# Kernel tuning notes

Hardware: AMD Instinct MI355X
Metric: run time of the kernel (lower is better)

## Reference

```python
import jax, jax.numpy as jnp
import numpy as np

N0, N1, N2 = 60000, 30000, 15000
E1, E2 = 960000, 480000
G, D, C = 2000, 400, 20
S0, S1, S2 = 1000, 1500, 2000  # gene index slice boundaries (shared/human/mouse)
EPS = 1e-5


def setup_inputs() -> dict:
    key = jax.random.key(0)
    ks = jax.random.split(key, 30)
    def lin(k, o, i):
        return (jax.random.normal(k, (o, i), jnp.float32) / np.sqrt(i)).astype(jnp.float32)
    inp = {}
    inp['x'] = jax.random.normal(ks[0], (N0, G), jnp.float32)
    inp['w_all'] = jax.random.uniform(ks[1], (E1 + E2, 1), jnp.float32)
    inp['W_sh'] = lin(ks[2], D, 1000); inp['b_sh'] = 0.01 * jax.random.normal(ks[3], (D,), jnp.float32)
    inp['W_hu'] = lin(ks[4], D, 500);  inp['b_hu'] = 0.01 * jax.random.normal(ks[5], (D,), jnp.float32)
    inp['W_mo'] = lin(ks[6], D, 500);  inp['b_mo'] = 0.01 * jax.random.normal(ks[7], (D,), jnp.float32)
    inp['Wn1'] = lin(ks[8], D, D);     inp['bn1'] = 0.01 * jax.random.normal(ks[9], (D,), jnp.float32)
    inp['Wn2'] = lin(ks[10], D, D);    inp['bn2'] = 0.01 * jax.random.normal(ks[11], (D,), jnp.float32)
    inp['W_lin'] = lin(ks[12], C, D);  inp['b_lin'] = 0.01 * jax.random.normal(ks[13], (C,), jnp.float32)
    inp['Wd1'] = lin(ks[14], 50, D);   inp['bd1'] = 0.01 * jax.random.normal(ks[15], (50,), jnp.float32)
    inp['gamma'] = jnp.ones((50,), jnp.float32)
    inp['beta'] = jnp.zeros((50,), jnp.float32)
    inp['Wd2'] = lin(ks[16], 2, 50);   inp['bd2'] = 0.01 * jax.random.normal(ks[17], (2,), jnp.float32)
    inp['src1'] = jax.random.randint(ks[18], (E1,), 0, N0)
    inp['dst1'] = jax.random.randint(ks[19], (E1,), 0, N1)
    inp['eid1'] = jax.random.randint(ks[20], (E1,), 0, E1 + E2)
    inp['src2'] = jax.random.randint(ks[21], (E2,), 0, N1)
    inp['dst2'] = jax.random.randint(ks[22], (E2,), 0, N2)
    inp['eid2'] = jax.random.randint(ks[23], (E2,), 0, E1 + E2)
    return inp


@jax.custom_vjp
def grad_reverse(x):
    return x

def _gr_fwd(x):
    return x, None

def _gr_bwd(_, g):
    return (-g,)  # ReverseLayerF with alpha=1

grad_reverse.defvjp(_gr_fwd, _gr_bwd)


def _gnn_layer(h_src, n_dst, src, dst, w_e, W, b):
    # weighted message gather-sum + degree-normalized self-combine (GNNConv)
    h_dst = h_src[:n_dst]
    m = h_src[src] * w_e                                   # [E, D]
    neigh = jax.ops.segment_sum(m, dst, num_segments=n_dst)
    deg = jax.ops.segment_sum(jnp.ones(dst.shape, h_src.dtype), dst, num_segments=n_dst)
    h_neigh = (neigh + h_dst) / (deg[:, None] + 1.0)
    return h_neigh @ W.T + b


def reference(x, w_all, W_sh, b_sh, W_hu, b_hu, W_mo, b_mo, Wn1, bn1, Wn2, bn2,
              W_lin, b_lin, Wd1, bd1, gamma, beta, Wd2, bd2,
              src1, dst1, eid1, src2, dst2, eid2):
    # one-hot selection matmuls == column slices of x, then three embeddings summed (FineGrainedLayerF)
    h = ((x[:, :S0] @ W_sh.T + b_sh)
         + (x[:, S0:S1] @ W_hu.T + b_hu)
         + (x[:, S1:S2] @ W_mo.T + b_mo))
    h1 = _gnn_layer(h, N1, src1, dst1, w_all[eid1], Wn1, bn1)
    h2 = _gnn_layer(h1, N2, src2, dst2, w_all[eid2], Wn2, bn2)
    h_x = h2 @ W_lin.T + b_lin
    # domain classifier on gradient-reversed features (BatchNorm1d in training mode)
    d = grad_reverse(h2) @ Wd1.T + bd1
    mu = jnp.mean(d, axis=0)
    var = jnp.var(d, axis=0)
    d = (d - mu) / jnp.sqrt(var + EPS) * gamma + beta
    d = jax.nn.relu(d)
    domain_x = d @ Wd2.T + bd2
    return (h_x, domain_x)
```

## Files before the change

kernel.cpp:

```cpp
#include <hip/hip_runtime.h>
#include <stdint.h>
#include <stddef.h>

typedef short bf16x8 __attribute__((ext_vector_type(8)));
typedef unsigned short ushort8 __attribute__((ext_vector_type(8)));
typedef float f32x4 __attribute__((ext_vector_type(4)));

__device__ __forceinline__ unsigned short f2bf(float f) {
  union { float f; unsigned int u; } v; v.f = f;
  unsigned int r = v.u + 0x7FFFu + ((v.u >> 16) & 1u);
  return (unsigned short)(r >> 16);
}
__device__ __forceinline__ float bf2f(unsigned short u) {
  union { unsigned int u; float f; } v; v.u = ((unsigned int)u) << 16; return v.f;
}

#define PAD 96

__global__ void prep_frag(
    const float* __restrict__ Wsh, const float* __restrict__ Whu, const float* __restrict__ Wmo,
    const float* __restrict__ Wn1, const float* __restrict__ Wn2,
    const float* __restrict__ Wlin, const float* __restrict__ Wd1,
    unsigned short* __restrict__ WCf, unsigned short* __restrict__ WN1f,
    unsigned short* __restrict__ WN2f, unsigned short* __restrict__ WHf,
    const float* __restrict__ bsh, const float* __restrict__ bhu, const float* __restrict__ bmo,
    const float* __restrict__ blin, const float* __restrict__ bd1,
    float* __restrict__ b3, float* __restrict__ bhead)
{
  const int NB_FRAG = 6784;
  const int bid = blockIdx.x;
  const int tid = threadIdx.x;
  if (bid < NB_FRAG) {
    const int s0 = 64 * 16384, s1 = s0 + 14 * 16384, s2 = s1 + 14 * 16384;
    int idx = bid * 256 + tid;
    int mode, rel;
    unsigned short* out;
    if (idx < s0)      { mode = 0; rel = idx;      out = WCf;  }
    else if (idx < s1) { mode = 1; rel = idx - s0; out = WN1f; }
    else if (idx < s2) { mode = 3; rel = idx - s1; out = WN2f; }
    else               { mode = 2; rel = idx - s2; out = WHf;  }
    int t = rel >> 14;
    int rem = rel & 16383;
    int e = rem & 7;
    int chunk = rem >> 3;
    int lane = chunk & 63;
    int g = chunk >> 6;
    int col = g * 16 + (lane & 15);
    int k = t * 32 + ((lane >> 4) << 3) + e;
    float v = 0.f;
    if (mode == 0) {
      if (col < 400 && k < 2000) {
        if (k < 1000)      v = Wsh[col * 1000 + k];
        else if (k < 1500) v = Whu[col * 500 + (k - 1000)];
        else               v = Wmo[col * 500 + (k - 1500)];
      }
    } else if (mode == 1) {
      if (col < 400 && k < 400) v = Wn1[col * 400 + k];
    } else if (mode == 3) {
      if (col < 400 && k < 400) v = Wn2[col * 400 + k];
    } else {
      if (k < 400) {
        if (col < 20)      v = Wlin[col * 400 + k];
        else if (col < 70) v = Wd1[(col - 20) * 400 + k];
      }
    }
    out[rel] = f2bf(v);
  } else {
    for (int t = tid; t < 512; t += 256) {
      if (t < 416) b3[t] = (t < 400) ? (bsh[t] + bhu[t] + bmo[t]) : 0.f;
      bhead[t] = (t < 20) ? blin[t] : ((t < 70) ? bd1[t - 20] : 0.f);
    }
  }
}

__global__ __launch_bounds__(256, 2) void gemm_stage1_adj(
    const float* __restrict__ Af, const unsigned short* __restrict__ Bf,
    const float* __restrict__ bias, unsigned short* __restrict__ C,
    int M, int Kreal, int ksteps, int NGEMM,
    const int* __restrict__ dst1, const int* __restrict__ src1, const int* __restrict__ eid1,
    int* __restrict__ cnt1, int* __restrict__ esrcP1, float* __restrict__ ewP1, int E1,
    const int* __restrict__ dst2, const int* __restrict__ src2, const int* __restrict__ eid2,
    int* __restrict__ cnt2, int* __restrict__ esrcP2, float* __restrict__ ewP2, int E2,
    const float* __restrict__ wall)
{
  __shared__ unsigned short As[2][64][36];

  if (blockIdx.x >= NGEMM) {
    int e = (blockIdx.x - NGEMM) * 256 + threadIdx.x;
    if (e < E1) {
      int d = dst1[e];
      int pos = atomicAdd(&cnt1[d], 1);
      if (pos < PAD) {
        esrcP1[d * PAD + pos] = src1[e];
        ewP1[d * PAD + pos] = wall[eid1[e]];
      }
    } else if (e < E1 + E2) {
      int e2 = e - E1;
      int d = dst2[e2];
      int pos = atomicAdd(&cnt2[d], 1);
      if (pos < PAD) {
        esrcP2[d * PAD + pos] = src2[e2];
        ewP2[d * PAD + pos] = wall[eid2[e2]];
      }
    }
    return;
  }

  const int tid = threadIdx.x;
  const int lane = tid & 63;
  const int wc = tid >> 6;
  const int rowBase = blockIdx.x * 64;
  const int sRow = tid >> 2;
  const int sC = (tid & 3) << 3;
  const int aRow = rowBase + sRow;
  const bool aOK = aRow < M;
  const int fr = lane & 15;
  const int fq = lane >> 4;

  const unsigned short* bWave = Bf + ((size_t)(wc * 8) * 64 + lane) * 8;

  f32x4 acc[4][8] = {};
  f32x4 a0lo, a0hi, a1lo, a1hi;
  bf16x8 bb[8];

  auto loadB = [&](int t) {
    const unsigned short* bp = bWave + (size_t)t * 16384;
    #pragma unroll
    for (int ni = 0; ni < 8; ++ni) bb[ni] = *(const bf16x8*)(bp + ni * 512);
  };
  auto loadA0 = [&](int t) {
    const int k0 = t * 32 + sC;
    if (aOK && (k0 + 4) <= Kreal) a0lo = *(const f32x4*)(Af + (size_t)aRow * Kreal + k0);
    else { a0lo[0]=0.f; a0lo[1]=0.f; a0lo[2]=0.f; a0lo[3]=0.f; }
    if (aOK && (k0 + 8) <= Kreal) a0hi = *(const f32x4*)(Af + (size_t)aRow * Kreal + k0 + 4);
    else { a0hi[0]=0.f; a0hi[1]=0.f; a0hi[2]=0.f; a0hi[3]=0.f; }
  };
  auto loadA1 = [&](int t) {
    const int k0 = t * 32 + sC;
    if (aOK && (k0 + 4) <= Kreal) a1lo = *(const f32x4*)(Af + (size_t)aRow * Kreal + k0);
    else { a1lo[0]=0.f; a1lo[1]=0.f; a1lo[2]=0.f; a1lo[3]=0.f; }
    if (aOK && (k0 + 8) <= Kreal) a1hi = *(const f32x4*)(Af + (size_t)aRow * Kreal + k0 + 4);
    else { a1hi[0]=0.f; a1hi[1]=0.f; a1hi[2]=0.f; a1hi[3]=0.f; }
  };
  auto writeA0 = [&](int buf) {
    ushort8 w;
    w[0]=f2bf(a0lo[0]); w[1]=f2bf(a0lo[1]); w[2]=f2bf(a0lo[2]); w[3]=f2bf(a0lo[3]);
    w[4]=f2bf(a0hi[0]); w[5]=f2bf(a0hi[1]); w[6]=f2bf(a0hi[2]); w[7]=f2bf(a0hi[3]);
    *(ushort8*)&As[buf][sRow][sC] = w;
  };
  auto writeA1 = [&](int buf) {
    ushort8 w;
    w[0]=f2bf(a1lo[0]); w[1]=f2bf(a1lo[1]); w[2]=f2bf(a1lo[2]); w[3]=f2bf(a1lo[3]);
    w[4]=f2bf(a1hi[0]); w[5]=f2bf(a1hi[1]); w[6]=f2bf(a1hi[2]); w[7]=f2bf(a1hi[3]);
    *(ushort8*)&As[buf][sRow][sC] = w;
  };
  auto compute = [&](int buf) {
    bf16x8 af[4];
    #pragma unroll
    for (int mi = 0; mi < 4; ++mi)
      af[mi] = *(const bf16x8*)&As[buf][(mi << 4) + fr][fq << 3];
    #pragma unroll
    for (int ni = 0; ni < 8; ++ni)
      #pragma unroll
      for (int mi = 0; mi < 4; ++mi)
        acc[mi][ni] = __builtin_amdgcn_mfma_f32_16x16x32_bf16(af[mi], bb[ni], acc[mi][ni], 0, 0, 0);
  };

  const int ksm1 = ksteps - 1;
  loadA0(0);
  loadB(0);
  loadA1(1 < ksm1 ? 1 : ksm1);
  writeA0(0);
  __syncthreads();
  loadA0(2 < ksm1 ? 2 : ksm1);

  for (int t = 0; t + 1 < ksteps; t += 2) {
    compute(0);
    loadB(t + 1);
    writeA1(1);
    __syncthreads();
    loadA1(t + 3 < ksm1 ? t + 3 : ksm1);
    compute(1);
    loadB(t + 2 < ksm1 ? t + 2 : ksm1);
    writeA0(0);
    __syncthreads();
    loadA0(t + 4 < ksm1 ? t + 4 : ksm1);
  }
  compute(0);

  #pragma unroll
  for (int mi = 0; mi < 4; ++mi) {
    const int row0 = rowBase + (mi << 4) + (fq << 2);
    #pragma unroll
    for (int ni = 0; ni < 8; ++ni) {
      const int col = (wc << 7) + (ni << 4) + fr;
      if (col < 416) {
        const float bv = (col < 400) ? bias[col] : 0.f;
        #pragma unroll
        for (int r = 0; r < 4; ++r) {
          const int row = row0 + r;
          if (row < M) C[(size_t)row * 416 + col] =
              (col < 400) ? f2bf(acc[mi][ni][r] + bv) : (unsigned short)0;
        }
      }
    }
  }
}

template<int HEAD, int ROWS>
__global__ __launch_bounds__(512) void fused_layer(
    const unsigned short* __restrict__ hsrc, const int* __restrict__ deg,
    const int* __restrict__ esrcP, const float* __restrict__ ewP,
    const unsigned short* __restrict__ Bf, const float* __restrict__ bias,
    unsigned short* __restrict__ Cout,
    const unsigned short* __restrict__ BfH, const float* __restrict__ biasH,
    float* __restrict__ outHx, float* __restrict__ dRaw, float* __restrict__ stats, int nDst)
{
  constexpr int MI = ROWS / 16;
  constexpr int NPW = ROWS / 8;
  __shared__ unsigned short T[ROWS][456];
  const int tid = threadIdx.x;
  const int lane = tid & 63;
  const int wv = tid >> 6;
  const int rowBase = blockIdx.x * ROWS;
  const int fr = lane & 15;
  const int fq = lane >> 4;

  for (int i = 0; i < NPW; ++i) {
    const int row = wv * NPW + i;
    const int node = rowBase + row;
    if (lane < 52) {
      float a[8];
      if (node < nDst) {
        ushort8 v = *(const ushort8*)(hsrc + (size_t)node * 416 + lane * 8);
        #pragma unroll
        for (int j = 0; j < 8; ++j) a[j] = bf2f(v[j]);
        int dg = deg[node]; if (dg > PAD) dg = PAD;
        const int e0 = node * PAD, e1 = e0 + dg;
        int e = e0;
        for (; e + 16 <= e1; e += 16) {
          int ss[16]; float ww[16];
          #pragma unroll
          for (int u = 0; u < 16; ++u) { ss[u] = esrcP[e + u]; ww[u] = ewP[e + u]; }
          ushort8 q0  = *(const ushort8*)(hsrc + (size_t)ss[0]  * 416 + lane * 8);
          ushort8 q1  = *(const ushort8*)(hsrc + (size_t)ss[1]  * 416 + lane * 8);
          ushort8 q2  = *(const ushort8*)(hsrc + (size_t)ss[2]  * 416 + lane * 8);
          ushort8 q3  = *(const ushort8*)(hsrc + (size_t)ss[3]  * 416 + lane * 8);
          ushort8 q4  = *(const ushort8*)(hsrc + (size_t)ss[4]  * 416 + lane * 8);
          ushort8 q5  = *(const ushort8*)(hsrc + (size_t)ss[5]  * 416 + lane * 8);
          ushort8 q6  = *(const ushort8*)(hsrc + (size_t)ss[6]  * 416 + lane * 8);
          ushort8 q7  = *(const ushort8*)(hsrc + (size_t)ss[7]  * 416 + lane * 8);
          ushort8 q8  = *(const ushort8*)(hsrc + (size_t)ss[8]  * 416 + lane * 8);
          ushort8 q9  = *(const ushort8*)(hsrc + (size_t)ss[9]  * 416 + lane * 8);
          ushort8 q10 = *(const ushort8*)(hsrc + (size_t)ss[10] * 416 + lane * 8);
          ushort8 q11 = *(const ushort8*)(hsrc + (size_t)ss[11] * 416 + lane * 8);
          ushort8 q12 = *(const ushort8*)(hsrc + (size_t)ss[12] * 416 + lane * 8);
          ushort8 q13 = *(const ushort8*)(hsrc + (size_t)ss[13] * 416 + lane * 8);
          ushort8 q14 = *(const ushort8*)(hsrc + (size_t)ss[14] * 416 + lane * 8);
          ushort8 q15 = *(const ushort8*)(hsrc + (size_t)ss[15] * 416 + lane * 8);
          #pragma unroll
          for (int j = 0; j < 8; ++j) {
            float p0 = (bf2f(q0[j])*ww[0] + bf2f(q1[j])*ww[1]) + (bf2f(q2[j])*ww[2] + bf2f(q3[j])*ww[3]);
            float p1 = (bf2f(q4[j])*ww[4] + bf2f(q5[j])*ww[5]) + (bf2f(q6[j])*ww[6] + bf2f(q7[j])*ww[7]);
            float p2 = (bf2f(q8[j])*ww[8] + bf2f(q9[j])*ww[9]) + (bf2f(q10[j])*ww[10] + bf2f(q11[j])*ww[11]);
            float p3 = (bf2f(q12[j])*ww[12] + bf2f(q13[j])*ww[13]) + (bf2f(q14[j])*ww[14] + bf2f(q15[j])*ww[15]);
            a[j] += (p0 + p1) + (p2 + p3);
          }
        }
        for (; e + 4 <= e1; e += 4) {
          const int s0 = esrcP[e], s1 = esrcP[e+1], s2 = esrcP[e+2], s3 = esrcP[e+3];
          const float w0 = ewP[e], w1 = ewP[e+1], w2 = ewP[e+2], w3 = ewP[e+3];
          ushort8 q0 = *(const ushort8*)(hsrc + (size_t)s0 * 416 + lane * 8);
          ushort8 q1 = *(const ushort8*)(hsrc + (size_t)s1 * 416 + lane * 8);
          ushort8 q2 = *(const ushort8*)(hsrc + (size_t)s2 * 416 + lane * 8);
          ushort8 q3 = *(const ushort8*)(hsrc + (size_t)s3 * 416 + lane * 8);
          #pragma unroll
          for (int j = 0; j < 8; ++j)
            a[j] += (bf2f(q0[j]) * w0 + bf2f(q1[j]) * w1) + (bf2f(q2[j]) * w2 + bf2f(q3[j]) * w3);
        }
        for (; e < e1; ++e) {
          const int s = esrcP[e];
          const float w = ewP[e];
          ushort8 q = *(const ushort8*)(hsrc + (size_t)s * 416 + lane * 8);
          #pragma unroll
          for (int j = 0; j < 8; ++j) a[j] += bf2f(q[j]) * w;
        }
        const float inv = 1.f / ((float)dg + 1.f);
        ushort8 o;
        #pragma unroll
        for (int j = 0; j < 8; ++j) o[j] = f2bf(a[j] * inv);
        *(ushort8*)&T[row][lane * 8] = o;
      } else {
        ushort8 o;
        #pragma unroll
        for (int j = 0; j < 8; ++j) o[j] = 0;
        *(ushort8*)&T[row][lane * 8] = o;
      }
    } else if (lane < 57) {
      ushort8 o;
      #pragma unroll
      for (int j = 0; j < 8; ++j) o[j] = 0;
      *(ushort8*)&T[row][416 + (lane - 52) * 8] = o;
    }
  }
  __syncthreads();

  const unsigned short* bWave = Bf + ((size_t)(wv * 4) * 64 + lane) * 8;
  f32x4 acc[MI][4] = {};
  bf16x8 bbA[4], bbB[4];

  auto loadBA = [&](int kh) {
    const unsigned short* bp = bWave + (size_t)kh * 16384;
    #pragma unroll
    for (int ni = 0; ni < 4; ++ni) bbA[ni] = *(const bf16x8*)(bp + ni * 512);
  };
  auto loadBB = [&](int kh) {
    const unsigned short* bp = bWave + (size_t)kh * 16384;
    #pragma unroll
    for (int ni = 0; ni < 4; ++ni) bbB[ni] = *(const bf16x8*)(bp + ni * 512);
  };
  auto computeA2 = [&](int kh) {
    bf16x8 af[MI];
    #pragma unroll
    for (int mi = 0; mi < MI; ++mi)
      af[mi] = *(const bf16x8*)&T[(mi << 4) + fr][kh * 32 + (fq << 3)];
    #pragma unroll
    for (int ni = 0; ni < 4; ++ni)
      #pragma unroll
      for (int mi = 0; mi < MI; ++mi)
        acc[mi][ni] = __builtin_amdgcn_mfma_f32_16x16x32_bf16(af[mi], bbA[ni], acc[mi][ni], 0, 0, 0);
  };
  auto computeB2 = [&](int kh) {
    bf16x8 af[MI];
    #pragma unroll
    for (int mi = 0; mi < MI; ++mi)
      af[mi] = *(const bf16x8*)&T[(mi << 4) + fr][kh * 32 + (fq << 3)];
    #pragma unroll
    for (int ni = 0; ni < 4; ++ni)
      #pragma unroll
      for (int mi = 0; mi < MI; ++mi)
        acc[mi][ni] = __builtin_amdgcn_mfma_f32_16x16x32_bf16(af[mi], bbB[ni], acc[mi][ni], 0, 0, 0);
  };

  loadBA(0);
  loadBB(1);
  for (int kh = 0; kh + 1 < 14; kh += 2) {
    computeA2(kh);
    loadBA(kh + 2 < 13 ? kh + 2 : 13);
    computeB2(kh + 1);
    loadBB(kh + 3 < 13 ? kh + 3 : 13);
  }

  if (HEAD == 0) {
    #pragma unroll
    for (int mi = 0; mi < MI; ++mi) {
      const int row0 = rowBase + (mi << 4) + (fq << 2);
      #pragma unroll
      for (int ni = 0; ni < 4; ++ni) {
        const int col = (wv << 6) + (ni << 4) + fr;
        if (col < 416) {
          const float bv = (col < 400) ? bias[col] : 0.f;
          #pragma unroll
          for (int r = 0; r < 4; ++r) {
            const int row = row0 + r;
            if (row < nDst) Cout[(size_t)row * 416 + col] =
                (col < 400) ? f2bf(acc[mi][ni][r] + bv) : (unsigned short)0;
          }
        }
      }
    }
  } else {
    __syncthreads();
    #pragma unroll
    for (int mi = 0; mi < MI; ++mi) {
      const int lrow0 = (mi << 4) + (fq << 2);
      #pragma unroll
      for (int ni = 0; ni < 4; ++ni) {
        const int col = (wv << 6) + (ni << 4) + fr;
        if (col < 456) {
          const float bv = (col < 400) ? bias[col] : 0.f;
          #pragma unroll
          for (int r = 0; r < 4; ++r)
            T[lrow0 + r][col] = (col < 400) ? f2bf(acc[mi][ni][r] + bv) : (unsigned short)0;
        }
      }
    }
    __syncthreads();
    const unsigned short* bhWave = BfH + ((size_t)wv * 64 + lane) * 8;
    f32x4 acc2[MI] = {};
    bf16x8 bhA, bhB;
    auto loadHA = [&](int kh) { bhA = *(const bf16x8*)(bhWave + (size_t)kh * 16384); };
    auto loadHB = [&](int kh) { bhB = *(const bf16x8*)(bhWave + (size_t)kh * 16384); };
    auto computeHA = [&](int kh) {
      #pragma unroll
      for (int mi = 0; mi < MI; ++mi) {
        bf16x8 af = *(const bf16x8*)&T[(mi << 4) + fr][kh * 32 + (fq << 3)];
        acc2[mi] = __builtin_amdgcn_mfma_f32_16x16x32_bf16(af, bhA, acc2[mi], 0, 0, 0);
      }
    };
    auto computeHB = [&](int kh) {
      #pragma unroll
      for (int mi = 0; mi < MI; ++mi) {
        bf16x8 af = *(const bf16x8*)&T[(mi << 4) + fr][kh * 32 + (fq << 3)];
        acc2[mi] = __builtin_amdgcn_mfma_f32_16x16x32_bf16(af, bhB, acc2[mi], 0, 0, 0);
      }
    };
    loadHA(0);
    loadHB(1);
    for (int kh = 0; kh + 1 < 14; kh += 2) {
      computeHA(kh);
      loadHA(kh + 2 < 13 ? kh + 2 : 13);
      computeHB(kh + 1);
      loadHB(kh + 3 < 13 ? kh + 3 : 13);
    }
    const int col = (wv << 4) + fr;
    const bool colOK = (col < 70);
    const float bv = colOK ? biasH[col] : 0.f;
    if (colOK) {
      #pragma unroll
      for (int mi = 0; mi < MI; ++mi) {
        const int row0 = rowBase + (mi << 4) + (fq << 2);
        #pragma unroll
        for (int r = 0; r < 4; ++r) {
          const int row = row0 + r;
          if (row < nDst) {
            float v = acc2[mi][r] + bv;
            if (col < 20) outHx[(size_t)row * 20 + col] = v;
            else          dRaw[(size_t)row * 50 + (col - 20)] = v;
          }
        }
      }
    }
    float s = 0.f, s2 = 0.f;
    if (col >= 20 && col < 70) {
      #pragma unroll
      for (int mi = 0; mi < MI; ++mi) {
        const int row0 = rowBase + (mi << 4) + (fq << 2);
        #pragma unroll
        for (int r = 0; r < 4; ++r) {
          if (row0 + r < nDst) {
            float v = acc2[mi][r] + bv;
            s += v; s2 += v * v;
          }
        }
      }
    }
    s  += __shfl_xor(s, 16);  s  += __shfl_xor(s, 32);
    s2 += __shfl_xor(s2, 16); s2 += __shfl_xor(s2, 32);
    if (col >= 20 && col < 70 && fq == 0) {
      atomicAdd(&stats[col - 20], s);
      atomicAdd(&stats[50 + col - 20], s2);
    }
  }
}

__global__ void domain_head2(const float* __restrict__ d, const float* __restrict__ stats,
                             const float* __restrict__ gamma, const float* __restrict__ beta,
                             const float* __restrict__ Wd2, const float* __restrict__ bd2,
                             float* __restrict__ out, int rows)
{
  __shared__ float ss[100];
  const int t = threadIdx.x;
  if (t < 50) {
    float mu = stats[t] / rows;
    float var = stats[50 + t] / rows - mu * mu;
    float inv = rsqrtf(var + 1e-5f);
    float sc = gamma[t] * inv;
    ss[t] = sc;
    ss[50 + t] = beta[t] - mu * sc;
  }
  __syncthreads();
  int r = blockIdx.x * 256 + t;
  if (r >= rows) return;
  float o0 = bd2[0], o1 = bd2[1];
  const float* dr = d + (size_t)r * 50;
  #pragma unroll 10
  for (int c = 0; c < 50; ++c) {
    float v = dr[c] * ss[c] + ss[50 + c];
    v = fmaxf(v, 0.f);
    o0 += v * Wd2[c];
    o1 += v * Wd2[50 + c];
  }
  out[r * 2]     = o0;
  out[r * 2 + 1] = o1;
}

extern "C" void kernel_launch(void* const* d_in, const int* in_sizes, int n_in,
                              void* d_out, int out_size, void* d_ws, size_t ws_size,
                              hipStream_t stream)
{
  const float* x    = (const float*)d_in[0];
  const float* wall = (const float*)d_in[1];
  const float* Wsh  = (const float*)d_in[2];
  const float* bsh  = (const float*)d_in[3];
  const float* Whu  = (const float*)d_in[4];
  const float* bhu  = (const float*)d_in[5];
  const float* Wmo  = (const float*)d_in[6];
  const float* bmo  = (const float*)d_in[7];
  const float* Wn1  = (const float*)d_in[8];
  const float* bn1  = (const float*)d_in[9];
  const float* Wn2  = (const float*)d_in[10];
  const float* bn2  = (const float*)d_in[11];
  const float* Wlin = (const float*)d_in[12];
  const float* blin = (const float*)d_in[13];
  const float* Wd1  = (const float*)d_in[14];
  const float* bd1  = (const float*)d_in[15];
  const float* gamma= (const float*)d_in[16];
  const float* beta = (const float*)d_in[17];
  const float* Wd2  = (const float*)d_in[18];
  const float* bd2  = (const float*)d_in[19];
  const int* src1 = (const int*)d_in[20];
  const int* dst1 = (const int*)d_in[21];
  const int* eid1 = (const int*)d_in[22];
  const int* src2 = (const int*)d_in[23];
  const int* dst2 = (const int*)d_in[24];
  const int* eid2 = (const int*)d_in[25];

  char* ws = (char*)d_ws;
  unsigned short* h    = (unsigned short*)(ws);
  unsigned short* h1   = (unsigned short*)(ws + 49920000ULL);
  float* d_raw         = (float*)(ws + 74880000ULL);
  unsigned short* WCf  = (unsigned short*)(ws + 77880000ULL);
  unsigned short* WN1f = (unsigned short*)(ws + 79977152ULL);
  unsigned short* WN2f = (unsigned short*)(ws + 80435904ULL);
  unsigned short* WHf  = (unsigned short*)(ws + 80894656ULL);
  float* b3      = (float*)(ws + 81353408ULL);
  float* bhead   = (float*)(ws + 81355456ULL);
  int*   cnt1    = (int*)(ws + 81357504ULL);
  int*   cnt2    = (int*)(ws + 81477504ULL);
  float* stats   = (float*)(ws + 81537504ULL);
  int*   esrcP1  = (int*)(ws + 81538304ULL);
  float* ewP1    = (float*)(ws + 93058304ULL);
  int*   esrcP2  = (int*)(ws + 104578304ULL);
  float* ewP2    = (float*)(ws + 110338304ULL);

  const int E1 = 960000, E2 = 480000;
  const int N0 = 60000, N1 = 30000, N2 = 15000;

  (void)hipMemsetAsync(cnt1, 0, 180400, stream);

  prep_frag<<<6785, 256, 0, stream>>>(
      Wsh, Whu, Wmo, Wn1, Wn2, Wlin, Wd1, WCf, WN1f, WN2f, WHf,
      bsh, bhu, bmo, blin, bd1, b3, bhead);

  gemm_stage1_adj<<<938 + 5625, 256, 0, stream>>>(
      x, WCf, b3, h, N0, 2000, 63, 938,
      dst1, src1, eid1, cnt1, esrcP1, ewP1, E1,
      dst2, src2, eid2, cnt2, esrcP2, ewP2, E2, wall);

  float* out_hx  = (float*)d_out;
  float* out_dom = (float*)d_out + 300000;

  fused_layer<0, 32><<<(N1 + 31) / 32, 512, 0, stream>>>(
      h, cnt1, esrcP1, ewP1, WN1f, bn1, h1, nullptr, nullptr, nullptr, nullptr, nullptr, N1);

  fused_layer<1, 32><<<(N2 + 31) / 32, 512, 0, stream>>>(
      h1, cnt2, esrcP2, ewP2, WN2f, bn2, nullptr, WHf, bhead, out_hx, d_raw, stats, N2);

  domain_head2<<<(N2 + 255) / 256, 256, 0, stream>>>(d_raw, stats, gamma, beta, Wd2, bd2, out_dom, N2);
}
```

Before: 529.2 us.

## Split stage-1 GEMM across 8 waves with smaller per-wave N tile

Raises the stage-1 GEMM block from 256 to 512 threads (8 waves). Each wave now owns 64 output columns instead of 128, which halves the per-thread accumulator and B-fragment registers and lets each thread load 4 A floats instead of 8. The edge-bucketing blocks are resized to 512 threads with a matching grid. The aim is higher occupancy and better latency hiding, in exchange for more waves sharing each A tile and more barrier participants per block.

```diff
diff --git a/kernel.cpp b/kernel.cpp
--- a/kernel.cpp
+++ b/kernel.cpp
@@ -4,6 +4,7 @@
 
 typedef short bf16x8 __attribute__((ext_vector_type(8)));
 typedef unsigned short ushort8 __attribute__((ext_vector_type(8)));
+typedef unsigned short usv4 __attribute__((ext_vector_type(4)));
 typedef float f32x4 __attribute__((ext_vector_type(4)));
 
 __device__ __forceinline__ unsigned short f2bf(float f) {
@@ -73,7 +74,7 @@
   }
 }
 
-__global__ __launch_bounds__(256, 2) void gemm_stage1_adj(
+__global__ __launch_bounds__(512, 4) void gemm_stage1_adj(
     const float* __restrict__ Af, const unsigned short* __restrict__ Bf,
     const float* __restrict__ bias, unsigned short* __restrict__ C,
     int M, int Kreal, int ksteps, int NGEMM,
@@ -86,7 +87,7 @@
   __shared__ unsigned short As[2][64][36];
 
   if (blockIdx.x >= NGEMM) {
-    int e = (blockIdx.x - NGEMM) * 256 + threadIdx.x;
+    int e = (blockIdx.x - NGEMM) * 512 + threadIdx.x;
     if (e < E1) {
       int d = dst1[e];
       int pos = atomicAdd(&cnt1[d], 1);
@@ -108,51 +109,45 @@
 
   const int tid = threadIdx.x;
   const int lane = tid & 63;
-  const int wc = tid >> 6;
+  const int wv = tid >> 6;
   const int rowBase = blockIdx.x * 64;
-  const int sRow = tid >> 2;
-  const int sC = (tid & 3) << 3;
+  const int sRow = tid >> 3;
+  const int sC = (tid & 7) << 2;
   const int aRow = rowBase + sRow;
   const bool aOK = aRow < M;
   const int fr = lane & 15;
   const int fq = lane >> 4;
 
-  const unsigned short* bWave = Bf + ((size_t)(wc * 8) * 64 + lane) * 8;
-
-  f32x4 acc[4][8] = {};
-  f32x4 a0lo, a0hi, a1lo, a1hi;
-  bf16x8 bb[8];
+  const unsigned short* bWave = Bf + ((size_t)(wv * 4) * 64 + lane) * 8;
+
+  f32x4 acc[4][4] = {};
+  f32x4 a0, a1;
+  bf16x8 bb[4];
 
   auto loadB = [&](int t) {
     const unsigned short* bp = bWave + (size_t)t * 16384;
     #pragma unroll
-    for (int ni = 0; ni < 8; ++ni) bb[ni] = *(const bf16x8*)(bp + ni * 512);
+    for (int ni = 0; ni < 4; ++ni) bb[ni] = *(const bf16x8*)(bp + ni * 512);
   };
   auto loadA0 = [&](int t) {
     const int k0 = t * 32 + sC;
-    if (aOK && (k0 + 4) <= Kreal) a0lo = *(const f32x4*)(Af + (size_t)aRow * Kreal + k0);
-    else { a0lo[0]=0.f; a0lo[1]=0.f; a0lo[2]=0.f; a0lo[3]=0.f; }
-    if (aOK && (k0 + 8) <= Kreal) a0hi = *(const f32x4*)(Af + (size_t)aRow * Kreal + k0 + 4);
-    else { a0hi[0]=0.f; a0hi[1]=0.f; a0hi[2]=0.f; a0hi[3]=0.f; }
+    if (aOK && (k0 + 4) <= Kreal) a0 = *(const f32x4*)(Af + (size_t)aRow * Kreal + k0);
+    else { a0[0]=0.f; a0[1]=0.f; a0[2]=0.f; a0[3]=0.f; }
   };
   auto loadA1 = [&](int t) {
     const int k0 = t * 32 + sC;
-    if (aOK && (k0 + 4) <= Kreal) a1lo = *(const f32x4*)(Af + (size_t)aRow * Kreal + k0);
-    else { a1lo[0]=0.f; a1lo[1]=0.f; a1lo[2]=0.f; a1lo[3]=0.f; }
-    if (aOK && (k0 + 8) <= Kreal) a1hi = *(const f32x4*)(Af + (size_t)aRow * Kreal + k0 + 4);
-    else { a1hi[0]=0.f; a1hi[1]=0.f; a1hi[2]=0.f; a1hi[3]=0.f; }
+    if (aOK && (k0 + 4) <= Kreal) a1 = *(const f32x4*)(Af + (size_t)aRow * Kreal + k0);
+    else { a1[0]=0.f; a1[1]=0.f; a1[2]=0.f; a1[3]=0.f; }
   };
   auto writeA0 = [&](int buf) {
-    ushort8 w;
-    w[0]=f2bf(a0lo[0]); w[1]=f2bf(a0lo[1]); w[2]=f2bf(a0lo[2]); w[3]=f2bf(a0lo[3]);
-    w[4]=f2bf(a0hi[0]); w[5]=f2bf(a0hi[1]); w[6]=f2bf(a0hi[2]); w[7]=f2bf(a0hi[3]);
-    *(ushort8*)&As[buf][sRow][sC] = w;
+    usv4 w;
+    w[0]=f2bf(a0[0]); w[1]=f2bf(a0[1]); w[2]=f2bf(a0[2]); w[3]=f2bf(a0[3]);
+    *(usv4*)&As[buf][sRow][sC] = w;
   };
   auto writeA1 = [&](int buf) {
-    ushort8 w;
-    w[0]=f2bf(a1lo[0]); w[1]=f2bf(a1lo[1]); w[2]=f2bf(a1lo[2]); w[3]=f2bf(a1lo[3]);
-    w[4]=f2bf(a1hi[0]); w[5]=f2bf(a1hi[1]); w[6]=f2bf(a1hi[2]); w[7]=f2bf(a1hi[3]);
-    *(ushort8*)&As[buf][sRow][sC] = w;
+    usv4 w;
+    w[0]=f2bf(a1[0]); w[1]=f2bf(a1[1]); w[2]=f2bf(a1[2]); w[3]=f2bf(a1[3]);
+    *(usv4*)&As[buf][sRow][sC] = w;
   };
   auto compute = [&](int buf) {
     bf16x8 af[4];
@@ -160,7 +155,7 @@
     for (int mi = 0; mi < 4; ++mi)
       af[mi] = *(const bf16x8*)&As[buf][(mi << 4) + fr][fq << 3];
     #pragma unroll
-    for (int ni = 0; ni < 8; ++ni)
+    for (int ni = 0; ni < 4; ++ni)
       #pragma unroll
       for (int mi = 0; mi < 4; ++mi)
         acc[mi][ni] = __builtin_amdgcn_mfma_f32_16x16x32_bf16(af[mi], bb[ni], acc[mi][ni], 0, 0, 0);
@@ -192,8 +187,8 @@
   for (int mi = 0; mi < 4; ++mi) {
     const int row0 = rowBase + (mi << 4) + (fq << 2);
     #pragma unroll
-    for (int ni = 0; ni < 8; ++ni) {
-      const int col = (wc << 7) + (ni << 4) + fr;
+    for (int ni = 0; ni < 4; ++ni) {
+      const int col = (wv << 6) + (ni << 4) + fr;
       if (col < 416) {
         const float bv = (col < 400) ? bias[col] : 0.f;
         #pragma unroll
@@ -543,7 +538,7 @@
       Wsh, Whu, Wmo, Wn1, Wn2, Wlin, Wd1, WCf, WN1f, WN2f, WHf,
       bsh, bhu, bmo, blin, bd1, b3, bhead);
 
-  gemm_stage1_adj<<<938 + 5625, 256, 0, stream>>>(
+  gemm_stage1_adj<<<938 + 2813, 512, 0, stream>>>(
       x, WCf, b3, h, N0, 2000, 63, 938,
       dst1, src1, eid1, cnt1, esrcP1, ewP1, E1,
       dst2, src2, eid2, cnt2, esrcP2, ewP2, E2, wall);
```

After: 500.4 us. 1.06x faster.
